# Kernel tuning notes

Measured on AMD Instinct MI355X. Metric: run time of the kernel, lower is better.

## Reference

```python
import jax, jax.numpy as jnp
import numpy as np

N = 1000000          # total nodes (events)
F = 64               # node feature dim
E = 4000000          # total edges
NB = 16              # number of graphs in batch
GRID = 64            # voxels per spatial dim; voxel_size = 1/GRID over [0,1)^2
VOXEL_SIZE = 1.0 / GRID
S = NB * GRID * GRID # fixed cluster-id space (batch-major voxel ids)


def setup_inputs() -> dict:
    key = jax.random.key(0)
    k1, k2, k3, k4 = jax.random.split(key, 4)
    x = jax.random.normal(k1, (N, F), dtype=jnp.float32)
    pos = jax.random.uniform(k2, (N, 2), dtype=jnp.float32)
    batch = jnp.sort(jax.random.randint(k3, (N,), 0, NB, dtype=jnp.int32))
    edge_index = jax.random.randint(k4, (2, E), 0, N, dtype=jnp.int32)
    return {"x": x, "pos": pos, "batch": batch, "edge_index": edge_index}


def reference(x, pos, batch, edge_index):
    # ---- voxel_grid: hash each node into a (batch, vy, vx) voxel cluster ----
    start = pos.min(axis=0)                                   # PyG uses global min as grid origin
    vox = jnp.clip(jnp.floor((pos - start) / VOXEL_SIZE).astype(jnp.int32), 0, GRID - 1)
    cluster = batch * (GRID * GRID) + vox[:, 1] * GRID + vox[:, 0]   # [N]

    # ---- max_pool: scatter-max features, scatter-mean positions ----
    x_pool = jax.ops.segment_max(x, cluster, num_segments=S)         # [S, F]
    count = jax.ops.segment_sum(jnp.ones((x.shape[0],), x.dtype), cluster, num_segments=S)
    node_valid = count > 0                                           # empty voxels masked
    x_pool = jnp.where(node_valid[:, None], x_pool, 0.0)
    pos_pool = jax.ops.segment_sum(pos, cluster, num_segments=S) / jnp.maximum(count, 1.0)[:, None]

    # ---- edge coarsening: map to clusters, drop self-loops, coalesce dups ----
    c_row = cluster[edge_index[0]]
    c_col = cluster[edge_index[1]]
    order = jnp.lexsort((c_col, c_row))                              # sort pairs (row primary)
    r = c_row[order]
    c = c_col[order]
    first = jnp.concatenate([jnp.array([True]), (r[1:] != r[:-1]) | (c[1:] != c[:-1])])
    edge_valid = first & (r != c)                                    # dedup + remove self-loops
    e_row = jnp.where(edge_valid, r, 0)
    e_col = jnp.where(edge_valid, c, 0)

    # ---- transform = Cartesian(norm=True, cat=False) on pooled positions ----
    cart = pos_pool[e_row] - pos_pool[e_col]                         # [E, 2]
    cart = jnp.where(edge_valid[:, None], cart, 0.0)
    max_val = jnp.max(jnp.abs(cart))
    edge_attr = jnp.where(edge_valid[:, None], cart / (2.0 * max_val) + 0.5, 0.0)

    return x_pool, pos_pool, jnp.stack([e_row, e_col]), edge_attr, edge_valid
```

## Files before the change

kernel.cpp:

```cpp
#include <hip/hip_runtime.h>
#include <math.h>

static constexpr int F     = 64;
static constexpr int GRIDV = 64;
static constexpr int SEG   = 16 * GRIDV * GRIDV;
static constexpr int MINB  = 256;
static constexpr int GPART = 512;
static constexpr int PTHR  = 512;
static constexpr int NBIN  = 512;
static constexpr int BSH   = 23;
static constexpr int ETBL  = NBIN * GPART;
static constexpr int SCAP  = 10240;
static constexpr int NGP   = 512;
static constexpr int NTH   = 256;
static constexpr int NTBL  = NBIN * NGP;
static constexpr int JTBL  = NTBL + ETBL;

typedef float __attribute__((ext_vector_type(4))) f32x4;

__device__ __forceinline__ float wave_min(float v) {
    for (int o = 32; o > 0; o >>= 1) v = fminf(v, __shfl_down(v, o));
    return v;
}
__device__ __forceinline__ float wave_max(float v) {
    for (int o = 32; o > 0; o >>= 1) v = fmaxf(v, __shfl_down(v, o));
    return v;
}
__device__ __forceinline__ f32x4 vmax4(f32x4 a, f32x4 b) {
    f32x4 r;
    r.x = fmaxf(a.x, b.x); r.y = fmaxf(a.y, b.y);
    r.z = fmaxf(a.z, b.z); r.w = fmaxf(a.w, b.w);
    return r;
}

template <int NT>
__device__ __forceinline__ unsigned block_incl_scan(unsigned v, int t) {
    __shared__ unsigned wsum[NT / 64];
    int lane = t & 63, w = t >> 6;
    unsigned sc = v;
    #pragma unroll
    for (int o = 1; o < 64; o <<= 1) {
        unsigned u = __shfl_up(sc, o);
        if (lane >= o) sc += u;
    }
    if (lane == 63) wsum[w] = sc;
    __syncthreads();
    if (w == 0 && lane < NT / 64) {
        unsigned ws = wsum[lane];
        #pragma unroll
        for (int o = 1; o < NT / 64; o <<= 1) {
            unsigned u = __shfl_up(ws, o);
            if (lane >= o) ws += u;
        }
        wsum[lane] = ws;
    }
    __syncthreads();
    return sc + ((w > 0) ? wsum[w - 1] : 0u);
}

__global__ void k_hdrinit(unsigned* hdr) {
    hdr[0] = 0x7F800000u;
    hdr[1] = 0x7F800000u;
}

__global__ void k_min(const float2* __restrict__ pos, int n, unsigned* hdr) {
    __shared__ float shx[4], shy[4];
    int stride = gridDim.x * blockDim.x;
    float mx = INFINITY, my = INFINITY;
    for (int i = blockIdx.x * blockDim.x + threadIdx.x; i < n; i += stride) {
        float2 p = pos[i];
        mx = fminf(mx, p.x); my = fminf(my, p.y);
    }
    mx = wave_min(mx); my = wave_min(my);
    int w = threadIdx.x >> 6;
    if ((threadIdx.x & 63) == 0) { shx[w] = mx; shy[w] = my; }
    __syncthreads();
    if (threadIdx.x == 0) {
        mx = fminf(fminf(shx[0], shx[1]), fminf(shx[2], shx[3]));
        my = fminf(fminf(shy[0], shy[1]), fminf(shy[2], shy[3]));
        atomicMin((int*)&hdr[0], __float_as_int(mx));
        atomicMin((int*)&hdr[1], __float_as_int(my));
    }
}

__global__ __launch_bounds__(NTH) void k_cluster(const float2* __restrict__ pos,
                          const int* __restrict__ batch, int n,
                          const unsigned* __restrict__ hdr, int* __restrict__ cl,
                          unsigned* __restrict__ ntable) {
    __shared__ unsigned hist[NBIN];
    int t = threadIdx.x, b = blockIdx.x;
    for (int j = t; j < NBIN; j += NTH) hist[j] = 0u;
    __syncthreads();
    float sx = __int_as_float((int)hdr[0]);
    float sy = __int_as_float((int)hdr[1]);
    for (int i = b * NTH + t; i < n; i += NGP * NTH) {
        float2 p = pos[i];
        int vx = min(max((int)floorf((p.x - sx) * 64.0f), 0), GRIDV - 1);
        int vy = min(max((int)floorf((p.y - sy) * 64.0f), 0), GRIDV - 1);
        int c = batch[i] * (GRIDV * GRIDV) + vy * GRIDV + vx;
        cl[i] = c;
        atomicAdd(&hist[(unsigned)c >> 7], 1u);
    }
    __syncthreads();
    for (int j = t; j < NBIN; j += NTH) ntable[j * NGP + b] = hist[j];
}

__global__ __launch_bounds__(PTHR) void k_ehist(const int* __restrict__ ei, int e,
                        const int* __restrict__ cl,
                        unsigned* __restrict__ keysA, unsigned* __restrict__ etbl) {
    __shared__ unsigned hist[NBIN];
    int t = threadIdx.x, b = blockIdx.x;
    for (int j = t; j < NBIN; j += PTHR) hist[j] = 0u;
    __syncthreads();
    for (int i = b * PTHR + t; i < e; i += GPART * PTHR) {
        unsigned r = (unsigned)cl[ei[i]];
        unsigned c = (unsigned)cl[ei[e + i]];
        unsigned k = (r << 16) | c;
        keysA[i] = k;
        atomicAdd(&hist[k >> BSH], 1u);
    }
    __syncthreads();
    for (int j = t; j < NBIN; j += PTHR) etbl[j * GPART + b] = hist[j];
}

__global__ void k_scan1(const unsigned* __restrict__ cnt, unsigned* __restrict__ off,
                        unsigned* __restrict__ blksum) {
    int t = threadIdx.x;
    int g = blockIdx.x * 1024 + t;
    unsigned v = cnt[g];
    unsigned incl = block_incl_scan<1024>(v, t);
    off[g] = incl - v;
    if (t == 1023) blksum[blockIdx.x] = incl;
}

__global__ void k_scan_add(unsigned* __restrict__ off, const unsigned* __restrict__ blksum,
                           int nblk, int nent, unsigned total) {
    __shared__ unsigned sh[512];
    int t = threadIdx.x, b = blockIdx.x;
    if (t < 512) sh[t] = (t < b && t < nblk) ? blksum[t] : 0u;
    __syncthreads();
    for (int s = 256; s > 0; s >>= 1) {
        if (t < s) sh[t] += sh[t + s];
        __syncthreads();
    }
    off[b * 1024 + t] += sh[0];
    if (b == 0 && t == 0) off[nent] = total;
}

__global__ __launch_bounds__(NTH) void k_npart(const int* __restrict__ cl,
                       const float2* __restrict__ pos, int n,
                       const unsigned* __restrict__ ntable,
                       unsigned* __restrict__ pc, unsigned* __restrict__ pn,
                       float2* __restrict__ ppos) {
    __shared__ unsigned stage_c[2048], stage_n[2048];
    __shared__ float stage_px[2048], stage_py[2048];
    __shared__ unsigned h[NBIN], cur[NBIN], tbl_s[NBIN];
    int t = threadIdx.x, b = blockIdx.x;
    for (int j = t; j < NBIN; j += NTH) {
        unsigned a = ntable[j * NGP + b];
        tbl_s[j] = a;
        h[j] = ntable[j * NGP + b + 1] - a;
    }
    __syncthreads();
    unsigned a0 = h[2 * t], a1 = h[2 * t + 1];
    unsigned incl = block_incl_scan<NTH>(a0 + a1, t);
    unsigned base = incl - (a0 + a1);
    cur[2 * t] = base;
    cur[2 * t + 1] = base + a0;
    __syncthreads();
    for (int i = b * NTH + t; i < n; i += NGP * NTH) {
        unsigned c = (unsigned)cl[i];
        float2 p = pos[i];
        unsigned q = atomicAdd(&cur[c >> 7], 1u);
        stage_c[q] = c; stage_n[q] = (unsigned)i;
        stage_px[q] = p.x; stage_py[q] = p.y;
    }
    __syncthreads();
    int cnt = (int)cur[NBIN - 1];
    for (int j = t; j < cnt; j += NTH) {
        unsigned c = stage_c[j];
        unsigned bin = c >> 7;
        unsigned start = cur[bin] - h[bin];
        unsigned g = tbl_s[bin] + ((unsigned)j - start);
        pc[g] = c; pn[g] = stage_n[j];
        ppos[g] = make_float2(stage_px[j], stage_py[j]);
    }
}

__global__ __launch_bounds__(256) void k_ngroup(const unsigned* __restrict__ pc,
                         const unsigned* __restrict__ pn, const float2* __restrict__ ppos,
                         const unsigned* __restrict__ ntable, int n,
                         unsigned* __restrict__ node_off, int* __restrict__ node_sorted,
                         float2* __restrict__ out_pos) {
    __shared__ unsigned cnt[128], sc[128], cur[128];
    __shared__ float psx[128], psy[128];
    int b = blockIdx.x, t = threadIdx.x;
    if (t < 128) { cnt[t] = 0u; psx[t] = 0.f; psy[t] = 0.f; }
    __syncthreads();
    int beg = (int)ntable[b * NGP];
    int end = (int)ntable[(b + 1) * NGP];
    for (int i = beg + t; i < end; i += 256) {
        unsigned c = pc[i] & 127u;
        float2 p = ppos[i];
        atomicAdd(&cnt[c], 1u);
        atomicAdd(&psx[c], p.x);
        atomicAdd(&psy[c], p.y);
    }
    __syncthreads();
    if (t < 128) sc[t] = cnt[t];
    __syncthreads();
    for (int s = 1; s < 128; s <<= 1) {
        unsigned u = (t >= s && t < 128) ? sc[t - s] : 0u;
        __syncthreads();
        if (t < 128) sc[t] += u;
        __syncthreads();
    }
    if (t < 128) {
        unsigned basec = (unsigned)beg + sc[t] - cnt[t];
        node_off[b * 128 + t] = basec;
        cur[t] = basec;
        unsigned c2 = cnt[t];
        out_pos[b * 128 + t] = c2 ? make_float2(psx[t] / (float)c2, psy[t] / (float)c2)
                                  : make_float2(0.f, 0.f);
    }
    if (b == NBIN - 1 && t == 0) node_off[SEG] = (unsigned)n;
    __syncthreads();
    for (int i = beg + t; i < end; i += 256) {
        unsigned c = pc[i] & 127u;
        unsigned slot = atomicAdd(&cur[c], 1u);
        node_sorted[slot] = (int)pn[i];
    }
}

__global__ __launch_bounds__(256) void k_pool(const float* __restrict__ x,
                      const int* __restrict__ node_sorted, const unsigned* __restrict__ off,
                      float* __restrict__ out_x) {
    int wid  = threadIdx.x >> 6;
    int lane = threadIdx.x & 63;
    int s = blockIdx.x * 4 + wid;
    unsigned beg = off[s], end = off[s + 1];
    int g   = lane >> 4;
    int cl4 = (lane & 15) << 2;
    f32x4 m0, m1, m2, m3;
    m0.x = m0.y = m0.z = m0.w = -INFINITY;
    m1 = m0; m2 = m0; m3 = m0;
    for (unsigned base = beg; base < end; base += 64) {
        int m = (int)min(64u, end - base);
        int nd_my = (lane < m) ? node_sorted[base + lane] : 0;
        int last = m - 1;
        int K = (m + 15) >> 4;
        for (int k = 0; k < K; ++k) {
            int j = g + (k << 4);
            int j0 = min(j, last);
            int j1 = min(j + 4, last);
            int j2 = min(j + 8, last);
            int j3 = min(j + 12, last);
            int n0 = __shfl(nd_my, j0);
            int n1 = __shfl(nd_my, j1);
            int n2 = __shfl(nd_my, j2);
            int n3 = __shfl(nd_my, j3);
            f32x4 v0 = __builtin_nontemporal_load((const f32x4*)&x[(size_t)n0 * F + cl4]);
            f32x4 v1 = __builtin_nontemporal_load((const f32x4*)&x[(size_t)n1 * F + cl4]);
            f32x4 v2 = __builtin_nontemporal_load((const f32x4*)&x[(size_t)n2 * F + cl4]);
            f32x4 v3 = __builtin_nontemporal_load((const f32x4*)&x[(size_t)n3 * F + cl4]);
            m0 = vmax4(m0, v0);
            m1 = vmax4(m1, v1);
            m2 = vmax4(m2, v2);
            m3 = vmax4(m3, v3);
        }
    }
    m0 = vmax4(vmax4(m0, m1), vmax4(m2, m3));
    #pragma unroll
    for (int o = 16; o <= 32; o <<= 1) {
        m0.x = fmaxf(m0.x, __shfl_xor(m0.x, o));
        m0.y = fmaxf(m0.y, __shfl_xor(m0.y, o));
        m0.z = fmaxf(m0.z, __shfl_xor(m0.z, o));
        m0.w = fmaxf(m0.w, __shfl_xor(m0.w, o));
    }
    if (g == 0) {
        f32x4 r;
        if (end > beg) r = m0;
        else { r.x = r.y = r.z = r.w = 0.f; }
        *(f32x4*)&out_x[(size_t)s * F + cl4] = r;
    }
}

__global__ __launch_bounds__(PTHR) void k_partition(const unsigned* __restrict__ keysA, int e,
                            const unsigned* __restrict__ etbl, unsigned bias,
                            unsigned* __restrict__ keysB) {
    __shared__ unsigned stage[8192];
    __shared__ unsigned h[NBIN], cur[NBIN], tbl_s[NBIN];
    int t = threadIdx.x, b = blockIdx.x;
    unsigned a = etbl[t * GPART + b] - bias;
    unsigned hv = (etbl[t * GPART + b + 1] - bias) - a;
    tbl_s[t] = a;
    h[t] = hv;
    __syncthreads();
    unsigned incl = block_incl_scan<PTHR>(hv, t);
    cur[t] = incl - hv;
    __syncthreads();
    for (int i = b * PTHR + t; i < e; i += GPART * PTHR) {
        unsigned k = keysA[i];
        unsigned p = atomicAdd(&cur[k >> BSH], 1u);
        stage[p] = k;
    }
    __syncthreads();
    int cnt = (int)cur[NBIN - 1];
    for (int j = t; j < cnt; j += PTHR) {
        unsigned k = stage[j];
        unsigned bin = k >> BSH;
        unsigned start = cur[bin] - h[bin];
        keysB[tbl_s[bin] + ((unsigned)j - start)] = k;
    }
}

__global__ __launch_bounds__(512) void k_subsort(const unsigned* __restrict__ src,
                         unsigned* __restrict__ dst, const unsigned* __restrict__ etbl,
                         unsigned bias, const float2* __restrict__ pos_pool,
                         float* __restrict__ pmax) {
    __shared__ unsigned hist[8192];
    __shared__ unsigned stage[SCAP];
    __shared__ float shm[8];
    int b = blockIdx.x, t = threadIdx.x;
    int beg = (int)(etbl[b * GPART] - bias);
    int end = (int)(etbl[(b + 1) * GPART] - bias);
    int len = end - beg;
    if (len <= 0) { if (t == 0) pmax[b] = 0.f; return; }
    for (int j = t; j < 8192; j += 512) hist[j] = 0u;
    __syncthreads();
    for (int i = beg + t; i < end; i += 512) {
        unsigned d = (src[i] >> 10) & 8191u;
        atomicAdd(&hist[((d & 15u) << 9) | (d >> 4)], 1u);
    }
    __syncthreads();
    unsigned loc[16];
    unsigned s = 0;
    #pragma unroll
    for (int u = 0; u < 16; ++u) { loc[u] = s; s += hist[u * 512 + t]; }
    unsigned incl = block_incl_scan<512>(s, t);
    bool inlds = (len <= SCAP);
    unsigned base0 = (inlds ? 0u : (unsigned)beg) + incl - s;
    #pragma unroll
    for (int u = 0; u < 16; ++u) hist[u * 512 + t] = base0 + loc[u];
    __syncthreads();
    float am = 0.f;
    if (inlds) {
        for (int i = beg + t; i < end; i += 512) {
            unsigned k = src[i];
            unsigned d = (k >> 10) & 8191u;
            stage[atomicAdd(&hist[((d & 15u) << 9) | (d >> 4)], 1u)] = k;
        }
        __syncthreads();
        for (int j = t; j < len; j += 512) {
            unsigned hi = stage[j] >> 10;
            if (j > 0 && (stage[j - 1] >> 10) == hi) continue;
            int rend = j + 1;
            while (rend < len && (stage[rend] >> 10) == hi) ++rend;
            for (int a2 = j + 1; a2 < rend; ++a2) {
                unsigned v = stage[a2]; int c = a2 - 1;
                while (c >= j && stage[c] > v) { stage[c + 1] = stage[c]; --c; }
                stage[c + 1] = v;
            }
        }
        __syncthreads();
        for (int j = t; j < len; j += 512) {
            unsigned k = stage[j];
            dst[beg + j] = k;
            bool first = (j == 0) || (stage[j - 1] != k);
            unsigned r = k >> 16, c = k & 0xFFFFu;
            if (first && r != c) {
                float2 pr = pos_pool[r], pcc = pos_pool[c];
                am = fmaxf(am, fmaxf(fabsf(pr.x - pcc.x), fabsf(pr.y - pcc.y)));
            }
        }
    } else {
        for (int i = beg + t; i < end; i += 512) {
            unsigned k = src[i];
            unsigned d = (k >> 10) & 8191u;
            dst[atomicAdd(&hist[((d & 15u) << 9) | (d >> 4)], 1u)] = k;
        }
        __threadfence();
        __syncthreads();
        for (int j = beg + t; j < end; j += 512) {
            unsigned hi = dst[j] >> 10;
            if (j > beg && (dst[j - 1] >> 10) == hi) continue;
            int rend = j + 1;
            while (rend < end && (dst[rend] >> 10) == hi) ++rend;
            for (int a2 = j + 1; a2 < rend; ++a2) {
                unsigned v = dst[a2]; int c = a2 - 1;
                while (c >= j && dst[c] > v) { dst[c + 1] = dst[c]; --c; }
                dst[c + 1] = v;
            }
        }
        __threadfence();
        __syncthreads();
        for (int j = beg + t; j < end; j += 512) {
            unsigned k = dst[j];
            bool first = (j == beg) || (dst[j - 1] != k);
            unsigned r = k >> 16, c = k & 0xFFFFu;
            if (first && r != c) {
                float2 pr = pos_pool[r], pcc = pos_pool[c];
                am = fmaxf(am, fmaxf(fabsf(pr.x - pcc.x), fabsf(pr.y - pcc.y)));
            }
        }
    }
    am = wave_max(am);
    if ((t & 63) == 0) shm[t >> 6] = am;
    __syncthreads();
    if (t == 0) {
        float m = shm[0];
        #pragma unroll
        for (int i2 = 1; i2 < 8; ++i2) m = fmaxf(m, shm[i2]);
        pmax[b] = m;
    }
}

__global__ __launch_bounds__(256) void k_eout(const unsigned* __restrict__ keys, int e,
                         const float2* __restrict__ pos_pool, const float* __restrict__ pmax,
                         float* __restrict__ out_erow, float* __restrict__ out_ecol,
                         float* __restrict__ out_valid, float2* __restrict__ out_attr) {
    __shared__ float shm[4];
    int t = threadIdx.x;
    float m = fmaxf(pmax[t], pmax[t + 256]);
    m = wave_max(m);
    if ((t & 63) == 0) shm[t >> 6] = m;
    __syncthreads();
    float denom = 2.0f * fmaxf(fmaxf(shm[0], shm[1]), fmaxf(shm[2], shm[3]));
    int i = blockIdx.x * blockDim.x + t;
    if (i >= e) return;
    unsigned k = keys[i];
    bool first = (i == 0) || (keys[i - 1] != k);
    unsigned r = k >> 16, c = k & 0xFFFFu;
    bool valid = first && (r != c);
    float ax = 0.f, ay = 0.f;
    if (valid) {
        float2 pr = pos_pool[r], pcc = pos_pool[c];
        ax = (pr.x - pcc.x) / denom + 0.5f;
        ay = (pr.y - pcc.y) / denom + 0.5f;
    }
    out_erow[i]  = valid ? (float)r : 0.f;
    out_ecol[i]  = valid ? (float)c : 0.f;
    out_valid[i] = valid ? 1.f : 0.f;
    out_attr[i]  = make_float2(ax, ay);
}

extern "C" void kernel_launch(void* const* d_in, const int* in_sizes, int n_in,
                              void* d_out, int out_size, void* d_ws, size_t ws_size,
                              hipStream_t stream) {
    const float* x    = (const float*)d_in[0];
    const float* pos  = (const float*)d_in[1];
    const int* batch  = (const int*)d_in[2];
    const int* ei     = (const int*)d_in[3];
    const int n = in_sizes[2];
    const int e = in_sizes[3] / 2;

    float* out      = (float*)d_out;
    float* out_x    = out;
    float* out_pos  = out_x  + (size_t)SEG * F;
    float* out_erow = out_pos + (size_t)SEG * 2;
    float* out_ecol = out_erow + e;
    float* out_attr = out_ecol + e;
    float* out_val  = out_attr + (size_t)2 * e;

    const int nb_e = (e + 255) / 256;

    char* w = (char*)d_ws;
    unsigned* hdr         = (unsigned*)w;
    int*      cl          = (int*)(w + 256);
    int*      node_sorted = (int*)(w + 256 + (size_t)n * 4);
    unsigned* node_off    = (unsigned*)(w + 256 + (size_t)n * 8);
    unsigned* table       = node_off + SEG + 1;
    unsigned* keysA       = table + JTBL + 1;
    unsigned* keysB       = keysA + e;
    unsigned* pc          = keysB + e;
    unsigned* pn          = pc + n;
    float2*   ppos        = (float2*)(pn + n);
    unsigned* blksum      = (unsigned*)(ppos + n);
    float*    pmax        = (float*)(blksum + 512);
    unsigned* ntable      = table;
    unsigned* etbl        = table + NTBL;

    k_hdrinit<<<1, 1, 0, stream>>>(hdr);
    k_min<<<MINB, 256, 0, stream>>>((const float2*)pos, n, hdr);
    k_cluster<<<NGP, NTH, 0, stream>>>((const float2*)pos, batch, n, hdr, cl, ntable);
    k_ehist<<<GPART, PTHR, 0, stream>>>(ei, e, cl, keysA, etbl);
    k_scan1<<<JTBL / 1024, 1024, 0, stream>>>(table, table, blksum);
    k_scan_add<<<JTBL / 1024, 1024, 0, stream>>>(table, blksum, JTBL / 1024, JTBL,
                                                 (unsigned)(n + e));
    k_npart<<<NGP, NTH, 0, stream>>>(cl, (const float2*)pos, n, ntable, pc, pn, ppos);
    k_ngroup<<<NBIN, 256, 0, stream>>>(pc, pn, ppos, ntable, n, node_off, node_sorted,
                                       (float2*)out_pos);
    k_partition<<<GPART, PTHR, 0, stream>>>(keysA, e, etbl, (unsigned)n, keysB);
    k_subsort<<<NBIN, 512, 0, stream>>>(keysB, keysA, etbl, (unsigned)n,
                                        (const float2*)out_pos, pmax);
    k_pool<<<SEG / 4, 256, 0, stream>>>(x, node_sorted, node_off, out_x);
    k_eout<<<nb_e, 256, 0, stream>>>(keysA, e, (const float2*)out_pos, pmax,
                                     out_erow, out_ecol, out_val, (float2*)out_attr);
}
```

Baseline: 248.9 us.

## Fuse all pooling and edge-coarsening stages into one persistent kernel with grid barriers

Replaces the chain of about a dozen separate kernel launches with a single persistent kernel of 256 blocks that runs every stage and uses a software grid barrier (atomic counter plus spin-wait) between stages. Each block handles two virtual partitions so the existing 512-way histogram, scan and partition layout is kept. The aim is to remove per-launch overhead and the idle tails between kernels. In exchange the grid barriers cost spin latency, occupancy is fixed at 256 blocks of 512 threads, and all co-resident blocks must be live at once or the kernel can deadlock.

```diff
diff --git a/kernel.cpp b/kernel.cpp
--- a/kernel.cpp
+++ b/kernel.cpp
@@ -4,17 +4,16 @@
 static constexpr int F     = 64;
 static constexpr int GRIDV = 64;
 static constexpr int SEG   = 16 * GRIDV * GRIDV;
-static constexpr int MINB  = 256;
-static constexpr int GPART = 512;
-static constexpr int PTHR  = 512;
+static constexpr int G     = 256;
+static constexpr int T     = 512;
+static constexpr int VB    = 512;
 static constexpr int NBIN  = 512;
 static constexpr int BSH   = 23;
-static constexpr int ETBL  = NBIN * GPART;
+static constexpr int NTBL  = NBIN * VB;
+static constexpr int ETBL  = NBIN * VB;
+static constexpr int JTBL  = NTBL + ETBL;
 static constexpr int SCAP  = 10240;
-static constexpr int NGP   = 512;
-static constexpr int NTH   = 256;
-static constexpr int NTBL  = NBIN * NGP;
-static constexpr int JTBL  = NTBL + ETBL;
+static constexpr int SMEMB = 57344;
 
 typedef float __attribute__((ext_vector_type(4))) f32x4;
 
@@ -58,390 +57,458 @@
     return sc + ((w > 0) ? wsum[w - 1] : 0u);
 }
 
-__global__ void k_hdrinit(unsigned* hdr) {
-    hdr[0] = 0x7F800000u;
-    hdr[1] = 0x7F800000u;
-}
-
-__global__ void k_min(const float2* __restrict__ pos, int n, unsigned* hdr) {
-    __shared__ float shx[4], shy[4];
-    int stride = gridDim.x * blockDim.x;
-    float mx = INFINITY, my = INFINITY;
-    for (int i = blockIdx.x * blockDim.x + threadIdx.x; i < n; i += stride) {
-        float2 p = pos[i];
-        mx = fminf(mx, p.x); my = fminf(my, p.y);
-    }
-    mx = wave_min(mx); my = wave_min(my);
-    int w = threadIdx.x >> 6;
-    if ((threadIdx.x & 63) == 0) { shx[w] = mx; shy[w] = my; }
+__device__ __forceinline__ void gbar(unsigned* bar, unsigned gen) {
     __syncthreads();
     if (threadIdx.x == 0) {
-        mx = fminf(fminf(shx[0], shx[1]), fminf(shx[2], shx[3]));
-        my = fminf(fminf(shy[0], shy[1]), fminf(shy[2], shy[3]));
-        atomicMin((int*)&hdr[0], __float_as_int(mx));
-        atomicMin((int*)&hdr[1], __float_as_int(my));
-    }
-}
-
-__global__ __launch_bounds__(NTH) void k_cluster(const float2* __restrict__ pos,
-                          const int* __restrict__ batch, int n,
-                          const unsigned* __restrict__ hdr, int* __restrict__ cl,
-                          unsigned* __restrict__ ntable) {
-    __shared__ unsigned hist[NBIN];
-    int t = threadIdx.x, b = blockIdx.x;
-    for (int j = t; j < NBIN; j += NTH) hist[j] = 0u;
+        __threadfence();
+        atomicAdd(bar, 1u);
+        unsigned target = gen * (unsigned)G;
+        while (__hip_atomic_load(bar, __ATOMIC_RELAXED, __HIP_MEMORY_SCOPE_AGENT) < target)
+            __builtin_amdgcn_s_sleep(2);
+        __threadfence();
+    }
     __syncthreads();
-    float sx = __int_as_float((int)hdr[0]);
-    float sy = __int_as_float((int)hdr[1]);
-    for (int i = b * NTH + t; i < n; i += NGP * NTH) {
-        float2 p = pos[i];
-        int vx = min(max((int)floorf((p.x - sx) * 64.0f), 0), GRIDV - 1);
-        int vy = min(max((int)floorf((p.y - sy) * 64.0f), 0), GRIDV - 1);
-        int c = batch[i] * (GRIDV * GRIDV) + vy * GRIDV + vx;
-        cl[i] = c;
-        atomicAdd(&hist[(unsigned)c >> 7], 1u);
-    }
-    __syncthreads();
-    for (int j = t; j < NBIN; j += NTH) ntable[j * NGP + b] = hist[j];
-}
-
-__global__ __launch_bounds__(PTHR) void k_ehist(const int* __restrict__ ei, int e,
-                        const int* __restrict__ cl,
-                        unsigned* __restrict__ keysA, unsigned* __restrict__ etbl) {
-    __shared__ unsigned hist[NBIN];
-    int t = threadIdx.x, b = blockIdx.x;
-    for (int j = t; j < NBIN; j += PTHR) hist[j] = 0u;
-    __syncthreads();
-    for (int i = b * PTHR + t; i < e; i += GPART * PTHR) {
-        unsigned r = (unsigned)cl[ei[i]];
-        unsigned c = (unsigned)cl[ei[e + i]];
-        unsigned k = (r << 16) | c;
-        keysA[i] = k;
-        atomicAdd(&hist[k >> BSH], 1u);
-    }
-    __syncthreads();
-    for (int j = t; j < NBIN; j += PTHR) etbl[j * GPART + b] = hist[j];
-}
-
-__global__ void k_scan1(const unsigned* __restrict__ cnt, unsigned* __restrict__ off,
-                        unsigned* __restrict__ blksum) {
-    int t = threadIdx.x;
-    int g = blockIdx.x * 1024 + t;
-    unsigned v = cnt[g];
-    unsigned incl = block_incl_scan<1024>(v, t);
-    off[g] = incl - v;
-    if (t == 1023) blksum[blockIdx.x] = incl;
-}
-
-__global__ void k_scan_add(unsigned* __restrict__ off, const unsigned* __restrict__ blksum,
-                           int nblk, int nent, unsigned total) {
-    __shared__ unsigned sh[512];
-    int t = threadIdx.x, b = blockIdx.x;
-    if (t < 512) sh[t] = (t < b && t < nblk) ? blksum[t] : 0u;
-    __syncthreads();
-    for (int s = 256; s > 0; s >>= 1) {
-        if (t < s) sh[t] += sh[t + s];
+}
+
+__global__ void k_binit(unsigned* bar) { *bar = 0u; }
+
+struct Args {
+    const float2* pos; const int* batch; const float* x; const int* ei;
+    int n, e;
+    unsigned* bar;
+    float2* pmin; unsigned* blksum;
+    int* cl; unsigned* table; unsigned* keysA; unsigned* keysB;
+    unsigned* pc; unsigned* pn; float2* ppos;
+    unsigned* node_off; int* node_sorted; float* pmax;
+    float* out_x; float2* out_pos;
+    float* out_erow; float* out_ecol; float* out_val; float2* out_attr;
+};
+
+__global__ __launch_bounds__(T, 2) void k_mega(Args a) {
+    __shared__ __align__(16) unsigned char SM[SMEMB];
+    __shared__ float s_red[16];
+    __shared__ unsigned s_tot;
+    const int b = blockIdx.x, t = threadIdx.x;
+    const int lane = t & 63, wid = t >> 6;
+    const int n = a.n, e = a.e;
+
+    {
+        float mx = INFINITY, my = INFINITY;
+        for (int k = 0; k < 8; ++k) {
+            int i = b * T + t + k * G * T;
+            if (i < n) { float2 p = a.pos[i]; mx = fminf(mx, p.x); my = fminf(my, p.y); }
+        }
+        mx = wave_min(mx); my = wave_min(my);
+        if (lane == 0) { s_red[wid] = mx; s_red[8 + wid] = my; }
         __syncthreads();
-    }
-    off[b * 1024 + t] += sh[0];
-    if (b == 0 && t == 0) off[nent] = total;
-}
-
-__global__ __launch_bounds__(NTH) void k_npart(const int* __restrict__ cl,
-                       const float2* __restrict__ pos, int n,
-                       const unsigned* __restrict__ ntable,
-                       unsigned* __restrict__ pc, unsigned* __restrict__ pn,
-                       float2* __restrict__ ppos) {
-    __shared__ unsigned stage_c[2048], stage_n[2048];
-    __shared__ float stage_px[2048], stage_py[2048];
-    __shared__ unsigned h[NBIN], cur[NBIN], tbl_s[NBIN];
-    int t = threadIdx.x, b = blockIdx.x;
-    for (int j = t; j < NBIN; j += NTH) {
-        unsigned a = ntable[j * NGP + b];
-        tbl_s[j] = a;
-        h[j] = ntable[j * NGP + b + 1] - a;
-    }
-    __syncthreads();
-    unsigned a0 = h[2 * t], a1 = h[2 * t + 1];
-    unsigned incl = block_incl_scan<NTH>(a0 + a1, t);
-    unsigned base = incl - (a0 + a1);
-    cur[2 * t] = base;
-    cur[2 * t + 1] = base + a0;
-    __syncthreads();
-    for (int i = b * NTH + t; i < n; i += NGP * NTH) {
-        unsigned c = (unsigned)cl[i];
-        float2 p = pos[i];
-        unsigned q = atomicAdd(&cur[c >> 7], 1u);
-        stage_c[q] = c; stage_n[q] = (unsigned)i;
-        stage_px[q] = p.x; stage_py[q] = p.y;
-    }
-    __syncthreads();
-    int cnt = (int)cur[NBIN - 1];
-    for (int j = t; j < cnt; j += NTH) {
-        unsigned c = stage_c[j];
-        unsigned bin = c >> 7;
-        unsigned start = cur[bin] - h[bin];
-        unsigned g = tbl_s[bin] + ((unsigned)j - start);
-        pc[g] = c; pn[g] = stage_n[j];
-        ppos[g] = make_float2(stage_px[j], stage_py[j]);
-    }
-}
-
-__global__ __launch_bounds__(256) void k_ngroup(const unsigned* __restrict__ pc,
-                         const unsigned* __restrict__ pn, const float2* __restrict__ ppos,
-                         const unsigned* __restrict__ ntable, int n,
-                         unsigned* __restrict__ node_off, int* __restrict__ node_sorted,
-                         float2* __restrict__ out_pos) {
-    __shared__ unsigned cnt[128], sc[128], cur[128];
-    __shared__ float psx[128], psy[128];
-    int b = blockIdx.x, t = threadIdx.x;
-    if (t < 128) { cnt[t] = 0u; psx[t] = 0.f; psy[t] = 0.f; }
-    __syncthreads();
-    int beg = (int)ntable[b * NGP];
-    int end = (int)ntable[(b + 1) * NGP];
-    for (int i = beg + t; i < end; i += 256) {
-        unsigned c = pc[i] & 127u;
-        float2 p = ppos[i];
-        atomicAdd(&cnt[c], 1u);
-        atomicAdd(&psx[c], p.x);
-        atomicAdd(&psy[c], p.y);
-    }
-    __syncthreads();
-    if (t < 128) sc[t] = cnt[t];
-    __syncthreads();
-    for (int s = 1; s < 128; s <<= 1) {
-        unsigned u = (t >= s && t < 128) ? sc[t - s] : 0u;
+        if (t == 0) {
+            for (int i = 1; i < 8; ++i) { mx = fminf(mx, s_red[i]); my = fminf(my, s_red[8 + i]); }
+            a.pmin[b] = make_float2(mx, my);
+        }
+    }
+    gbar(a.bar, 1);
+
+    {
+        float mxv = INFINITY, myv = INFINITY;
+        if (t < G) { float2 pp = a.pmin[t]; mxv = pp.x; myv = pp.y; }
+        mxv = wave_min(mxv); myv = wave_min(myv);
+        if (lane == 0) { s_red[wid] = mxv; s_red[8 + wid] = myv; }
         __syncthreads();
-        if (t < 128) sc[t] += u;
+        float sx = s_red[0], sy = s_red[8];
+        #pragma unroll
+        for (int i = 1; i < 8; ++i) { sx = fminf(sx, s_red[i]); sy = fminf(sy, s_red[8 + i]); }
         __syncthreads();
-    }
-    if (t < 128) {
-        unsigned basec = (unsigned)beg + sc[t] - cnt[t];
-        node_off[b * 128 + t] = basec;
-        cur[t] = basec;
-        unsigned c2 = cnt[t];
-        out_pos[b * 128 + t] = c2 ? make_float2(psx[t] / (float)c2, psy[t] / (float)c2)
-                                  : make_float2(0.f, 0.f);
-    }
-    if (b == NBIN - 1 && t == 0) node_off[SEG] = (unsigned)n;
-    __syncthreads();
-    for (int i = beg + t; i < end; i += 256) {
-        unsigned c = pc[i] & 127u;
-        unsigned slot = atomicAdd(&cur[c], 1u);
-        node_sorted[slot] = (int)pn[i];
-    }
-}
-
-__global__ __launch_bounds__(256) void k_pool(const float* __restrict__ x,
-                      const int* __restrict__ node_sorted, const unsigned* __restrict__ off,
-                      float* __restrict__ out_x) {
-    int wid  = threadIdx.x >> 6;
-    int lane = threadIdx.x & 63;
-    int s = blockIdx.x * 4 + wid;
-    unsigned beg = off[s], end = off[s + 1];
-    int g   = lane >> 4;
-    int cl4 = (lane & 15) << 2;
-    f32x4 m0, m1, m2, m3;
-    m0.x = m0.y = m0.z = m0.w = -INFINITY;
-    m1 = m0; m2 = m0; m3 = m0;
-    for (unsigned base = beg; base < end; base += 64) {
-        int m = (int)min(64u, end - base);
-        int nd_my = (lane < m) ? node_sorted[base + lane] : 0;
-        int last = m - 1;
-        int K = (m + 15) >> 4;
-        for (int k = 0; k < K; ++k) {
-            int j = g + (k << 4);
-            int j0 = min(j, last);
-            int j1 = min(j + 4, last);
-            int j2 = min(j + 8, last);
-            int j3 = min(j + 12, last);
-            int n0 = __shfl(nd_my, j0);
-            int n1 = __shfl(nd_my, j1);
-            int n2 = __shfl(nd_my, j2);
-            int n3 = __shfl(nd_my, j3);
-            f32x4 v0 = __builtin_nontemporal_load((const f32x4*)&x[(size_t)n0 * F + cl4]);
-            f32x4 v1 = __builtin_nontemporal_load((const f32x4*)&x[(size_t)n1 * F + cl4]);
-            f32x4 v2 = __builtin_nontemporal_load((const f32x4*)&x[(size_t)n2 * F + cl4]);
-            f32x4 v3 = __builtin_nontemporal_load((const f32x4*)&x[(size_t)n3 * F + cl4]);
-            m0 = vmax4(m0, v0);
-            m1 = vmax4(m1, v1);
-            m2 = vmax4(m2, v2);
-            m3 = vmax4(m3, v3);
-        }
-    }
-    m0 = vmax4(vmax4(m0, m1), vmax4(m2, m3));
-    #pragma unroll
-    for (int o = 16; o <= 32; o <<= 1) {
-        m0.x = fmaxf(m0.x, __shfl_xor(m0.x, o));
-        m0.y = fmaxf(m0.y, __shfl_xor(m0.y, o));
-        m0.z = fmaxf(m0.z, __shfl_xor(m0.z, o));
-        m0.w = fmaxf(m0.w, __shfl_xor(m0.w, o));
-    }
-    if (g == 0) {
-        f32x4 r;
-        if (end > beg) r = m0;
-        else { r.x = r.y = r.z = r.w = 0.f; }
-        *(f32x4*)&out_x[(size_t)s * F + cl4] = r;
-    }
-}
-
-__global__ __launch_bounds__(PTHR) void k_partition(const unsigned* __restrict__ keysA, int e,
-                            const unsigned* __restrict__ etbl, unsigned bias,
-                            unsigned* __restrict__ keysB) {
-    __shared__ unsigned stage[8192];
-    __shared__ unsigned h[NBIN], cur[NBIN], tbl_s[NBIN];
-    int t = threadIdx.x, b = blockIdx.x;
-    unsigned a = etbl[t * GPART + b] - bias;
-    unsigned hv = (etbl[t * GPART + b + 1] - bias) - a;
-    tbl_s[t] = a;
-    h[t] = hv;
-    __syncthreads();
-    unsigned incl = block_incl_scan<PTHR>(hv, t);
-    cur[t] = incl - hv;
-    __syncthreads();
-    for (int i = b * PTHR + t; i < e; i += GPART * PTHR) {
-        unsigned k = keysA[i];
-        unsigned p = atomicAdd(&cur[k >> BSH], 1u);
-        stage[p] = k;
-    }
-    __syncthreads();
-    int cnt = (int)cur[NBIN - 1];
-    for (int j = t; j < cnt; j += PTHR) {
-        unsigned k = stage[j];
-        unsigned bin = k >> BSH;
-        unsigned start = cur[bin] - h[bin];
-        keysB[tbl_s[bin] + ((unsigned)j - start)] = k;
-    }
-}
-
-__global__ __launch_bounds__(512) void k_subsort(const unsigned* __restrict__ src,
-                         unsigned* __restrict__ dst, const unsigned* __restrict__ etbl,
-                         unsigned bias, const float2* __restrict__ pos_pool,
-                         float* __restrict__ pmax) {
-    __shared__ unsigned hist[8192];
-    __shared__ unsigned stage[SCAP];
-    __shared__ float shm[8];
-    int b = blockIdx.x, t = threadIdx.x;
-    int beg = (int)(etbl[b * GPART] - bias);
-    int end = (int)(etbl[(b + 1) * GPART] - bias);
-    int len = end - beg;
-    if (len <= 0) { if (t == 0) pmax[b] = 0.f; return; }
-    for (int j = t; j < 8192; j += 512) hist[j] = 0u;
-    __syncthreads();
-    for (int i = beg + t; i < end; i += 512) {
-        unsigned d = (src[i] >> 10) & 8191u;
-        atomicAdd(&hist[((d & 15u) << 9) | (d >> 4)], 1u);
-    }
-    __syncthreads();
-    unsigned loc[16];
-    unsigned s = 0;
-    #pragma unroll
-    for (int u = 0; u < 16; ++u) { loc[u] = s; s += hist[u * 512 + t]; }
-    unsigned incl = block_incl_scan<512>(s, t);
-    bool inlds = (len <= SCAP);
-    unsigned base0 = (inlds ? 0u : (unsigned)beg) + incl - s;
-    #pragma unroll
-    for (int u = 0; u < 16; ++u) hist[u * 512 + t] = base0 + loc[u];
-    __syncthreads();
-    float am = 0.f;
-    if (inlds) {
-        for (int i = beg + t; i < end; i += 512) {
-            unsigned k = src[i];
-            unsigned d = (k >> 10) & 8191u;
-            stage[atomicAdd(&hist[((d & 15u) << 9) | (d >> 4)], 1u)] = k;
-        }
+        unsigned* hist = (unsigned*)SM;
+        for (int v = 0; v < 2; ++v) {
+            int vb = 2 * b + v;
+            hist[t] = 0u;
+            __syncthreads();
+            for (int k = 0; k < 4; ++k) {
+                int i = vb * T + t + k * VB * T;
+                if (i < n) {
+                    float2 p = a.pos[i];
+                    int vx = min(max((int)floorf((p.x - sx) * 64.0f), 0), GRIDV - 1);
+                    int vy = min(max((int)floorf((p.y - sy) * 64.0f), 0), GRIDV - 1);
+                    int c = a.batch[i] * (GRIDV * GRIDV) + vy * GRIDV + vx;
+                    a.cl[i] = c;
+                    atomicAdd(&hist[(unsigned)c >> 7], 1u);
+                }
+            }
+            __syncthreads();
+            a.table[t * VB + vb] = hist[t];
+            __syncthreads();
+        }
+    }
+    gbar(a.bar, 2);
+
+    {
+        unsigned* hist = (unsigned*)SM;
+        for (int v = 0; v < 2; ++v) {
+            int vb = 2 * b + v;
+            hist[t] = 0u;
+            __syncthreads();
+            for (int k = 0; k < 16; ++k) {
+                int i = vb * T + t + k * VB * T;
+                if (i < e) {
+                    unsigned r = (unsigned)a.cl[a.ei[i]];
+                    unsigned c = (unsigned)a.cl[a.ei[e + i]];
+                    unsigned kk = (r << 16) | c;
+                    a.keysA[i] = kk;
+                    atomicAdd(&hist[kk >> BSH], 1u);
+                }
+            }
+            __syncthreads();
+            a.table[NTBL + t * VB + vb] = hist[t];
+            __syncthreads();
+        }
+    }
+    gbar(a.bar, 3);
+
+    {
+        for (int v = 0; v < 2; ++v) {
+            int c = 2 * b + v;
+            int base = c * 1024;
+            unsigned v0 = a.table[base + t];
+            unsigned v1 = a.table[base + 512 + t];
+            unsigned i0 = block_incl_scan<T>(v0, t);
+            if (t == 511) s_tot = i0;
+            __syncthreads();
+            unsigned t0 = s_tot;
+            unsigned i1 = block_incl_scan<T>(v1, t) + t0;
+            a.table[base + t]       = i0 - v0;
+            a.table[base + 512 + t] = i1 - v1;
+            if (t == 511) a.blksum[c] = i1;
+            __syncthreads();
+        }
+    }
+    gbar(a.bar, 4);
+
+    {
+        unsigned* sh = (unsigned*)SM;
+        for (int v = 0; v < 2; ++v) {
+            int c = 2 * b + v;
+            int base = c * 1024;
+            sh[t] = (t < c) ? a.blksum[t] : 0u;
+            __syncthreads();
+            for (int s = 256; s > 0; s >>= 1) {
+                if (t < s) sh[t] += sh[t + s];
+                __syncthreads();
+            }
+            unsigned add = sh[0];
+            a.table[base + t]       += add;
+            a.table[base + 512 + t] += add;
+            __syncthreads();
+        }
+        if (b == 0 && t == 0) a.table[JTBL] = (unsigned)(n + e);
+    }
+    gbar(a.bar, 5);
+
+    {
+        unsigned* stage_c  = (unsigned*)SM;
+        unsigned* stage_n  = stage_c + 2048;
+        float*    stage_px = (float*)(stage_n + 2048);
+        float*    stage_py = stage_px + 2048;
+        unsigned* h    = (unsigned*)(stage_py + 2048);
+        unsigned* cur  = h + 512;
+        unsigned* tbl  = cur + 512;
+        for (int v = 0; v < 2; ++v) {
+            int vb = 2 * b + v;
+            unsigned aof = a.table[t * VB + vb];
+            unsigned hv  = a.table[t * VB + vb + 1] - aof;
+            tbl[t] = aof; h[t] = hv;
+            unsigned incl = block_incl_scan<T>(hv, t);
+            cur[t] = incl - hv;
+            __syncthreads();
+            for (int k = 0; k < 4; ++k) {
+                int i = vb * T + t + k * VB * T;
+                if (i < n) {
+                    unsigned c = (unsigned)a.cl[i];
+                    float2 p = a.pos[i];
+                    unsigned q = atomicAdd(&cur[c >> 7], 1u);
+                    stage_c[q] = c; stage_n[q] = (unsigned)i;
+                    stage_px[q] = p.x; stage_py[q] = p.y;
+                }
+            }
+            __syncthreads();
+            int cnt = (int)cur[NBIN - 1];
+            for (int j = t; j < cnt; j += T) {
+                unsigned c = stage_c[j];
+                unsigned bin = c >> 7;
+                unsigned start = cur[bin] - h[bin];
+                unsigned g2 = tbl[bin] + ((unsigned)j - start);
+                a.pc[g2] = c; a.pn[g2] = stage_n[j];
+                a.ppos[g2] = make_float2(stage_px[j], stage_py[j]);
+            }
+            __syncthreads();
+        }
+    }
+    gbar(a.bar, 6);
+
+    {
+        unsigned* cnt = (unsigned*)SM;
+        unsigned* sc  = cnt + 128;
+        unsigned* cur = sc + 128;
+        float* psx = (float*)(cur + 128);
+        float* psy = psx + 128;
+        for (int v = 0; v < 2; ++v) {
+            int vb = 2 * b + v;
+            if (t < 128) { cnt[t] = 0u; psx[t] = 0.f; psy[t] = 0.f; }
+            __syncthreads();
+            int beg = (int)a.table[vb * VB];
+            int end = (int)a.table[(vb + 1) * VB];
+            for (int i = beg + t; i < end; i += T) {
+                unsigned c = a.pc[i] & 127u;
+                float2 p = a.ppos[i];
+                atomicAdd(&cnt[c], 1u);
+                atomicAdd(&psx[c], p.x);
+                atomicAdd(&psy[c], p.y);
+            }
+            __syncthreads();
+            if (t < 128) sc[t] = cnt[t];
+            __syncthreads();
+            for (int s = 1; s < 128; s <<= 1) {
+                unsigned u = (t >= s && t < 128) ? sc[t - s] : 0u;
+                __syncthreads();
+                if (t < 128) sc[t] += u;
+                __syncthreads();
+            }
+            if (t < 128) {
+                unsigned basec = (unsigned)beg + sc[t] - cnt[t];
+                a.node_off[vb * 128 + t] = basec;
+                cur[t] = basec;
+                unsigned c2 = cnt[t];
+                a.out_pos[vb * 128 + t] = c2 ? make_float2(psx[t] / (float)c2, psy[t] / (float)c2)
+                                             : make_float2(0.f, 0.f);
+            }
+            if (vb == VB - 1 && t == 0) a.node_off[SEG] = (unsigned)n;
+            __syncthreads();
+            for (int i = beg + t; i < end; i += T) {
+                unsigned c = a.pc[i] & 127u;
+                unsigned slot = atomicAdd(&cur[c], 1u);
+                a.node_sorted[slot] = (int)a.pn[i];
+            }
+            __syncthreads();
+        }
+    }
+    {
+        unsigned* stg  = (unsigned*)SM;
+        unsigned* h    = stg + 8192;
+        unsigned* cur  = h + 512;
+        unsigned* tbl2 = cur + 512;
+        for (int v = 0; v < 2; ++v) {
+            int vb = 2 * b + v;
+            unsigned aof = a.table[NTBL + t * VB + vb] - (unsigned)n;
+            unsigned hv  = (a.table[NTBL + t * VB + vb + 1] - (unsigned)n) - aof;
+            tbl2[t] = aof; h[t] = hv;
+            unsigned incl = block_incl_scan<T>(hv, t);
+            cur[t] = incl - hv;
+            __syncthreads();
+            for (int k = 0; k < 16; ++k) {
+                int i = vb * T + t + k * VB * T;
+                if (i < e) {
+                    unsigned kk = a.keysA[i];
+                    unsigned p = atomicAdd(&cur[kk >> BSH], 1u);
+                    stg[p] = kk;
+                }
+            }
+            __syncthreads();
+            int cnt2 = (int)cur[NBIN - 1];
+            for (int j = t; j < cnt2; j += T) {
+                unsigned kk = stg[j];
+                unsigned bin = kk >> BSH;
+                unsigned start = cur[bin] - h[bin];
+                a.keysB[tbl2[bin] + ((unsigned)j - start)] = kk;
+            }
+            __syncthreads();
+        }
+    }
+    gbar(a.bar, 7);
+
+    {
+        unsigned* hist = (unsigned*)SM;
+        unsigned* stg  = (unsigned*)SM + 4096;
+        for (int v = 0; v < 2; ++v) {
+            int vb = 2 * b + v;
+            int beg = (int)(a.table[NTBL + vb * VB] - (unsigned)n);
+            int end = (int)(a.table[NTBL + (vb + 1) * VB] - (unsigned)n);
+            int len = end - beg;
+            float am = 0.f;
+            if (len > 0) {
+                for (int j = t; j < 4096; j += T) hist[j] = 0u;
+                __syncthreads();
+                for (int i = beg + t; i < end; i += T) {
+                    unsigned d = (a.keysB[i] >> 11) & 4095u;
+                    atomicAdd(&hist[((d & 7u) << 9) | (d >> 3)], 1u);
+                }
+                __syncthreads();
+                unsigned loc[8];
+                unsigned s = 0;
+                #pragma unroll
+                for (int u = 0; u < 8; ++u) { loc[u] = s; s += hist[u * 512 + t]; }
+                unsigned incl = block_incl_scan<T>(s, t);
+                bool inlds = (len <= SCAP);
+                unsigned base0 = (inlds ? 0u : (unsigned)beg) + incl - s;
+                #pragma unroll
+                for (int u = 0; u < 8; ++u) hist[u * 512 + t] = base0 + loc[u];
+                __syncthreads();
+                if (inlds) {
+                    for (int i = beg + t; i < end; i += T) {
+                        unsigned k = a.keysB[i];
+                        unsigned d = (k >> 11) & 4095u;
+                        stg[atomicAdd(&hist[((d & 7u) << 9) | (d >> 3)], 1u)] = k;
+                    }
+                    __syncthreads();
+                    for (int j = t; j < len; j += T) {
+                        unsigned hi = stg[j] >> 11;
+                        if (j > 0 && (stg[j - 1] >> 11) == hi) continue;
+                        int rend = j + 1;
+                        while (rend < len && (stg[rend] >> 11) == hi) ++rend;
+                        for (int a2 = j + 1; a2 < rend; ++a2) {
+                            unsigned vv = stg[a2]; int c = a2 - 1;
+                            while (c >= j && stg[c] > vv) { stg[c + 1] = stg[c]; --c; }
+                            stg[c + 1] = vv;
+                        }
+                    }
+                    __syncthreads();
+                    for (int j = t; j < len; j += T) {
+                        unsigned k = stg[j];
+                        a.keysA[beg + j] = k;
+                        bool first = (j == 0) || (stg[j - 1] != k);
+                        unsigned r = k >> 16, c = k & 0xFFFFu;
+                        if (first && r != c) {
+                            float2 pr = a.out_pos[r], pcc = a.out_pos[c];
+                            am = fmaxf(am, fmaxf(fabsf(pr.x - pcc.x), fabsf(pr.y - pcc.y)));
+                        }
+                    }
+                } else {
+                    for (int i = beg + t; i < end; i += T) {
+                        unsigned k = a.keysB[i];
+                        unsigned d = (k >> 11) & 4095u;
+                        a.keysA[atomicAdd(&hist[((d & 7u) << 9) | (d >> 3)], 1u)] = k;
+                    }
+                    __threadfence();
+                    __syncthreads();
+                    for (int j = beg + t; j < end; j += T) {
+                        unsigned hi = a.keysA[j] >> 11;
+                        if (j > beg && (a.keysA[j - 1] >> 11) == hi) continue;
+                        int rend = j + 1;
+                        while (rend < end && (a.keysA[rend] >> 11) == hi) ++rend;
+                        for (int a2 = j + 1; a2 < rend; ++a2) {
+                            unsigned vv = a.keysA[a2]; int c = a2 - 1;
+                            while (c >= j && a.keysA[c] > vv) { a.keysA[c + 1] = a.keysA[c]; --c; }
+                            a.keysA[c + 1] = vv;
+                        }
+                    }
+                    __threadfence();
+                    __syncthreads();
+                    for (int j = beg + t; j < end; j += T) {
+                        unsigned k = a.keysA[j];
+                        bool first = (j == beg) || (a.keysA[j - 1] != k);
+                        unsigned r = k >> 16, c = k & 0xFFFFu;
+                        if (first && r != c) {
+                            float2 pr = a.out_pos[r], pcc = a.out_pos[c];
+                            am = fmaxf(am, fmaxf(fabsf(pr.x - pcc.x), fabsf(pr.y - pcc.y)));
+                        }
+                    }
+                }
+            }
+            __syncthreads();
+            am = wave_max(am);
+            if (lane == 0) s_red[wid] = am;
+            __syncthreads();
+            if (t == 0) {
+                float m = s_red[0];
+                #pragma unroll
+                for (int i = 1; i < 8; ++i) m = fmaxf(m, s_red[i]);
+                a.pmax[vb] = m;
+            }
+            __syncthreads();
+        }
+    }
+    {
+        for (int v = 0; v < 2; ++v) {
+            int vb = 2 * b + v;
+            for (int k2 = 0; k2 < 16; ++k2) {
+                int s = vb * 128 + wid + 8 * k2;
+                unsigned pbeg = a.node_off[s], pend = a.node_off[s + 1];
+                int g2  = lane >> 4;
+                int cl4 = (lane & 15) << 2;
+                f32x4 m0, m1, m2, m3;
+                m0.x = m0.y = m0.z = m0.w = -INFINITY;
+                m1 = m0; m2 = m0; m3 = m0;
+                for (unsigned base2 = pbeg; base2 < pend; base2 += 64) {
+                    int m = (int)min(64u, pend - base2);
+                    int nd_my = (lane < m) ? a.node_sorted[base2 + lane] : 0;
+                    int last = m - 1;
+                    int K = (m + 15) >> 4;
+                    for (int k = 0; k < K; ++k) {
+                        int j = g2 + (k << 4);
+                        int j0 = min(j, last);
+                        int j1 = min(j + 4, last);
+                        int j2 = min(j + 8, last);
+                        int j3 = min(j + 12, last);
+                        int n0 = __shfl(nd_my, j0);
+                        int n1 = __shfl(nd_my, j1);
+                        int n2 = __shfl(nd_my, j2);
+                        int n3 = __shfl(nd_my, j3);
+                        f32x4 v0 = __builtin_nontemporal_load((const f32x4*)&a.x[(size_t)n0 * F + cl4]);
+                        f32x4 v1 = __builtin_nontemporal_load((const f32x4*)&a.x[(size_t)n1 * F + cl4]);
+                        f32x4 v2 = __builtin_nontemporal_load((const f32x4*)&a.x[(size_t)n2 * F + cl4]);
+                        f32x4 v3 = __builtin_nontemporal_load((const f32x4*)&a.x[(size_t)n3 * F + cl4]);
+                        m0 = vmax4(m0, v0);
+                        m1 = vmax4(m1, v1);
+                        m2 = vmax4(m2, v2);
+                        m3 = vmax4(m3, v3);
+                    }
+                }
+                m0 = vmax4(vmax4(m0, m1), vmax4(m2, m3));
+                #pragma unroll
+                for (int o = 16; o <= 32; o <<= 1) {
+                    m0.x = fmaxf(m0.x, __shfl_xor(m0.x, o));
+                    m0.y = fmaxf(m0.y, __shfl_xor(m0.y, o));
+                    m0.z = fmaxf(m0.z, __shfl_xor(m0.z, o));
+                    m0.w = fmaxf(m0.w, __shfl_xor(m0.w, o));
+                }
+                if (g2 == 0) {
+                    f32x4 r;
+                    if (pend > pbeg) r = m0;
+                    else { r.x = r.y = r.z = r.w = 0.f; }
+                    *(f32x4*)&a.out_x[(size_t)s * F + cl4] = r;
+                }
+            }
+        }
+    }
+    gbar(a.bar, 8);
+
+    {
+        float m = a.pmax[t];
+        m = wave_max(m);
+        if (lane == 0) s_red[wid] = m;
         __syncthreads();
-        for (int j = t; j < len; j += 512) {
-            unsigned hi = stage[j] >> 10;
-            if (j > 0 && (stage[j - 1] >> 10) == hi) continue;
-            int rend = j + 1;
-            while (rend < len && (stage[rend] >> 10) == hi) ++rend;
-            for (int a2 = j + 1; a2 < rend; ++a2) {
-                unsigned v = stage[a2]; int c = a2 - 1;
-                while (c >= j && stage[c] > v) { stage[c + 1] = stage[c]; --c; }
-                stage[c + 1] = v;
-            }
-        }
-        __syncthreads();
-        for (int j = t; j < len; j += 512) {
-            unsigned k = stage[j];
-            dst[beg + j] = k;
-            bool first = (j == 0) || (stage[j - 1] != k);
-            unsigned r = k >> 16, c = k & 0xFFFFu;
-            if (first && r != c) {
-                float2 pr = pos_pool[r], pcc = pos_pool[c];
-                am = fmaxf(am, fmaxf(fabsf(pr.x - pcc.x), fabsf(pr.y - pcc.y)));
-            }
-        }
-    } else {
-        for (int i = beg + t; i < end; i += 512) {
-            unsigned k = src[i];
-            unsigned d = (k >> 10) & 8191u;
-            dst[atomicAdd(&hist[((d & 15u) << 9) | (d >> 4)], 1u)] = k;
-        }
-        __threadfence();
-        __syncthreads();
-        for (int j = beg + t; j < end; j += 512) {
-            unsigned hi = dst[j] >> 10;
-            if (j > beg && (dst[j - 1] >> 10) == hi) continue;
-            int rend = j + 1;
-            while (rend < end && (dst[rend] >> 10) == hi) ++rend;
-            for (int a2 = j + 1; a2 < rend; ++a2) {
-                unsigned v = dst[a2]; int c = a2 - 1;
-                while (c >= j && dst[c] > v) { dst[c + 1] = dst[c]; --c; }
-                dst[c + 1] = v;
-            }
-        }
-        __threadfence();
-        __syncthreads();
-        for (int j = beg + t; j < end; j += 512) {
-            unsigned k = dst[j];
-            bool first = (j == beg) || (dst[j - 1] != k);
-            unsigned r = k >> 16, c = k & 0xFFFFu;
-            if (first && r != c) {
-                float2 pr = pos_pool[r], pcc = pos_pool[c];
-                am = fmaxf(am, fmaxf(fabsf(pr.x - pcc.x), fabsf(pr.y - pcc.y)));
-            }
-        }
-    }
-    am = wave_max(am);
-    if ((t & 63) == 0) shm[t >> 6] = am;
-    __syncthreads();
-    if (t == 0) {
-        float m = shm[0];
+        float dm = s_red[0];
         #pragma unroll
-        for (int i2 = 1; i2 < 8; ++i2) m = fmaxf(m, shm[i2]);
-        pmax[b] = m;
-    }
-}
-
-__global__ __launch_bounds__(256) void k_eout(const unsigned* __restrict__ keys, int e,
-                         const float2* __restrict__ pos_pool, const float* __restrict__ pmax,
-                         float* __restrict__ out_erow, float* __restrict__ out_ecol,
-                         float* __restrict__ out_valid, float2* __restrict__ out_attr) {
-    __shared__ float shm[4];
-    int t = threadIdx.x;
-    float m = fmaxf(pmax[t], pmax[t + 256]);
-    m = wave_max(m);
-    if ((t & 63) == 0) shm[t >> 6] = m;
-    __syncthreads();
-    float denom = 2.0f * fmaxf(fmaxf(shm[0], shm[1]), fmaxf(shm[2], shm[3]));
-    int i = blockIdx.x * blockDim.x + t;
-    if (i >= e) return;
-    unsigned k = keys[i];
-    bool first = (i == 0) || (keys[i - 1] != k);
-    unsigned r = k >> 16, c = k & 0xFFFFu;
-    bool valid = first && (r != c);
-    float ax = 0.f, ay = 0.f;
-    if (valid) {
-        float2 pr = pos_pool[r], pcc = pos_pool[c];
-        ax = (pr.x - pcc.x) / denom + 0.5f;
-        ay = (pr.y - pcc.y) / denom + 0.5f;
-    }
-    out_erow[i]  = valid ? (float)r : 0.f;
-    out_ecol[i]  = valid ? (float)c : 0.f;
-    out_valid[i] = valid ? 1.f : 0.f;
-    out_attr[i]  = make_float2(ax, ay);
+        for (int i = 1; i < 8; ++i) dm = fmaxf(dm, s_red[i]);
+        float denom = 2.0f * dm;
+        for (int k2 = 0; k2 < 32; ++k2) {
+            int i = b * T + t + k2 * G * T;
+            if (i < e) {
+                unsigned kk = a.keysA[i];
+                bool first = (i == 0) || (a.keysA[i - 1] != kk);
+                unsigned r = kk >> 16, c = kk & 0xFFFFu;
+                bool valid = first && (r != c);
+                float ax = 0.f, ay = 0.f;
+                if (valid) {
+                    float2 pr = a.out_pos[r], pcc = a.out_pos[c];
+                    ax = (pr.x - pcc.x) / denom + 0.5f;
+                    ay = (pr.y - pcc.y) / denom + 0.5f;
+                }
+                a.out_erow[i] = valid ? (float)r : 0.f;
+                a.out_ecol[i] = valid ? (float)c : 0.f;
+                a.out_val[i]  = valid ? 1.f : 0.f;
+                a.out_attr[i] = make_float2(ax, ay);
+            }
+        }
+    }
 }
 
 extern "C" void kernel_launch(void* const* d_in, const int* in_sizes, int n_in,
@@ -462,10 +529,8 @@
     float* out_attr = out_ecol + e;
     float* out_val  = out_attr + (size_t)2 * e;
 
-    const int nb_e = (e + 255) / 256;
-
     char* w = (char*)d_ws;
-    unsigned* hdr         = (unsigned*)w;
+    unsigned* bar         = (unsigned*)w;
     int*      cl          = (int*)(w + 256);
     int*      node_sorted = (int*)(w + 256 + (size_t)n * 4);
     unsigned* node_off    = (unsigned*)(w + 256 + (size_t)n * 8);
@@ -475,25 +540,22 @@
     unsigned* pc          = keysB + e;
     unsigned* pn          = pc + n;
     float2*   ppos        = (float2*)(pn + n);
-    unsigned* blksum      = (unsigned*)(ppos + n);
-    float*    pmax        = (float*)(blksum + 512);
-    unsigned* ntable      = table;
-    unsigned* etbl        = table + NTBL;
-
-    k_hdrinit<<<1, 1, 0, stream>>>(hdr);
-    k_min<<<MINB, 256, 0, stream>>>((const float2*)pos, n, hdr);
-    k_cluster<<<NGP, NTH, 0, stream>>>((const float2*)pos, batch, n, hdr, cl, ntable);
-    k_ehist<<<GPART, PTHR, 0, stream>>>(ei, e, cl, keysA, etbl);
-    k_scan1<<<JTBL / 1024, 1024, 0, stream>>>(table, table, blksum);
-    k_scan_add<<<JTBL / 1024, 1024, 0, stream>>>(table, blksum, JTBL / 1024, JTBL,
-                                                 (unsigned)(n + e));
-    k_npart<<<NGP, NTH, 0, stream>>>(cl, (const float2*)pos, n, ntable, pc, pn, ppos);
-    k_ngroup<<<NBIN, 256, 0, stream>>>(pc, pn, ppos, ntable, n, node_off, node_sorted,
-                                       (float2*)out_pos);
-    k_partition<<<GPART, PTHR, 0, stream>>>(keysA, e, etbl, (unsigned)n, keysB);
-    k_subsort<<<NBIN, 512, 0, stream>>>(keysB, keysA, etbl, (unsigned)n,
-                                        (const float2*)out_pos, pmax);
-    k_pool<<<SEG / 4, 256, 0, stream>>>(x, node_sorted, node_off, out_x);
-    k_eout<<<nb_e, 256, 0, stream>>>(keysA, e, (const float2*)out_pos, pmax,
-                                     out_erow, out_ecol, out_val, (float2*)out_attr);
-}
+    float2*   pmin        = (float2*)(ppos + n);
+    unsigned* blksum      = (unsigned*)(pmin + G);
+    float*    pmax        = (float*)(blksum + VB);
+
+    Args args;
+    args.pos = (const float2*)pos; args.batch = batch; args.x = x; args.ei = ei;
+    args.n = n; args.e = e;
+    args.bar = bar;
+    args.pmin = pmin; args.blksum = blksum;
+    args.cl = cl; args.table = table; args.keysA = keysA; args.keysB = keysB;
+    args.pc = pc; args.pn = pn; args.ppos = ppos;
+    args.node_off = node_off; args.node_sorted = node_sorted; args.pmax = pmax;
+    args.out_x = out_x; args.out_pos = (float2*)out_pos;
+    args.out_erow = out_erow; args.out_ecol = out_ecol; args.out_val = out_val;
+    args.out_attr = (float2*)out_attr;
+
+    k_binit<<<1, 1, 0, stream>>>(bar);
+    k_mega<<<G, T, 0, stream>>>(args);
+}
```

Measured after the change: 530.0 us. 2.13x slower.
